# Performance work log

Measured on AMD Instinct MI355X. Metric: run time of the kernel, lower is better.

The kernel has to match this reference:

```python
import jax, jax.numpy as jnp
import numpy as np

N_OUT = 4096
N_IN = 4096
FRAC_SPARSE = 0.5
N_SPARSE = int(FRAC_SPARSE * N_OUT * N_IN)  # 8388608
TOKENS = 256


def setup_inputs() -> dict:
    key = jax.random.key(0)
    k1, k2 = jax.random.split(key)
    # x: activations fed to F.linear
    x = jax.random.normal(k1, (TOKENS, N_IN), dtype=jnp.float32)
    # sparse_values: nn.Parameter of size n_sparse
    sparse_values = jax.random.normal(k2, (N_SPARSE,), dtype=jnp.float32) * 0.02
    # sparse_mask as sorted unique row-major flat indices of True entries.
    # torch `out[mask] = values` fills values into True positions in row-major
    # order, which equals scattering values at the ascending-sorted flat idxs.
    rng = np.random.default_rng(0)
    flat_idx = np.sort(rng.permutation(N_OUT * N_IN)[:N_SPARSE]).astype(np.int32)
    return {"x": x, "sparse_values": sparse_values, "flat_idx": jnp.asarray(flat_idx)}


def reference(x, sparse_values, flat_idx):
    # reconstruct(): dense [n_out, n_in] weight via scatter of sparse values
    W = (
        jnp.zeros((N_OUT * N_IN,), dtype=sparse_values.dtype)
        .at[flat_idx]
        .set(sparse_values)
        .reshape(N_OUT, N_IN)
    )
    # F.linear(x, W) == x @ W.T
    return x @ W.T
```

## Files before the change

### kernel.cpp

```cpp
#include <hip/hip_runtime.h>
#include <stdint.h>

#define N_OUT    4096
#define N_IN     4096
#define TOKENS   256
#define N_SPARSE 8388608
#define SPLITK   16
#define KCHUNK   256
#define NSEG     (N_IN / KCHUNK)
#define CPW      (NSEG + 1)
#define BN       64

typedef __attribute__((ext_vector_type(8))) short bf16x8;
typedef __attribute__((ext_vector_type(8))) unsigned short u16x8;
typedef __attribute__((ext_vector_type(4))) float f32x4;

__device__ __forceinline__ unsigned short f2bf(float f) {
    union { float f; unsigned u; } v; v.f = f;
    unsigned r = v.u + 0x7fffu + ((v.u >> 16) & 1u);
    return (unsigned short)(r >> 16);
}

__device__ __forceinline__ float bf2f(unsigned short u) {
    union { unsigned u; float f; } v; v.u = ((unsigned)u) << 16;
    return v.f;
}

__device__ __forceinline__ void ld4(const int* __restrict__ idx,
                                    const float* __restrict__ vals,
                                    int jb, int4& i4, float4& v4) {
    if (jb + 4 <= N_SPARSE) {
        i4 = *(const int4*)(idx + jb);
        v4 = *(const float4*)(vals + jb);
    } else {
        i4 = int4{0, 0, 0, 0}; v4 = float4{0.f, 0.f, 0.f, 0.f};
        #pragma unroll
        for (int e = 0; e < 4; ++e) {
            const int j = jb + e;
            if (j < N_SPARSE) { (&i4.x)[e] = idx[j]; (&v4.x)[e] = vals[j]; }
        }
    }
}

__global__ void prep(const float* __restrict__ x, const int* __restrict__ idx,
                     unsigned short* __restrict__ xs, int* __restrict__ cp) {
    const int b = blockIdx.x;
    const int t = threadIdx.x;
    if (b < 1024) {
        const int i = (b * 256 + t) * 4;
        const int m = i >> 12;
        const int k = i & 4095;
        const float4 v = *(const float4*)(x + i);
        ushort4 o;
        o.x = f2bf(v.x); o.y = f2bf(v.y); o.z = f2bf(v.z); o.w = f2bf(v.w);
        const int lane = (m & 15) | (((k >> 3) & 3) << 4);
        const int addr = ((k >> 5) * 16 + (m >> 4)) * 512 + lane * 8 + (k & 7);
        *(ushort4*)(xs + addr) = o;
    } else {
        const int e = (b - 1024) * 256 + t;
        const int r = e / CPW;
        const int z = e - r * CPW;
        const int target = r * N_IN + z * KCHUNK;
        int lo = 0, hi = N_SPARSE;
        while (lo < hi) { int m = (lo + hi) >> 1; if (idx[m] < target) lo = m + 1; else hi = m; }
        cp[e] = lo;
    }
}

__global__ __launch_bounds__(256) void fused_gemm(
        const unsigned short* __restrict__ xs,
        const int* __restrict__ idx,
        const float* __restrict__ vals,
        const int* __restrict__ cp,
        unsigned short* __restrict__ part)
{
    __shared__ short Bs[BN * KCHUNK];

    const int tid = threadIdx.x;
    const int l   = tid & 63;
    const int w   = tid >> 6;
    const int bn  = blockIdx.x;
    const int bz  = blockIdx.y;

    {
        const u16x8 z8 = {};
        unsigned short* b0 = (unsigned short*)Bs + tid * 64;
        #pragma unroll
        for (int q = 0; q < 8; ++q) *(u16x8*)(b0 + q * 8) = z8;
    }
    __syncthreads();

    {
        const int rl    = tid >> 2;
        const int sub   = tid & 3;
        const int rglob = bn * BN + rl;
        const int start = cp[rglob * CPW + bz];
        const int end   = cp[rglob * CPW + bz + 1];
        const int base  = rglob * N_IN + bz * KCHUNK;
        unsigned short* brow = (unsigned short*)Bs + rl * KCHUNK;
        const int rx = (rl & 7) << 3;

        int jb = (start & ~3) + sub * 4;
        int4 i4; float4 v4;
        bool have = jb < end;
        if (have) ld4(idx, vals, jb, i4, v4);
        while (have) {
            const int jn = jb + 16;
            const bool haven = jn < end;
            int4 i4n; float4 v4n;
            if (haven) ld4(idx, vals, jn, i4n, v4n);
            #pragma unroll
            for (int e = 0; e < 4; ++e) {
                const int j = jb + e;
                if (j >= start && j < end) {
                    const int cc = (&i4.x)[e] - base;
                    brow[((cc & ~7) ^ rx) | (cc & 7)] = f2bf((&v4.x)[e]);
                }
            }
            jb = jn; i4 = i4n; v4 = v4n; have = haven;
        }
    }
    __syncthreads();

    const int lr  = l & 15;
    const int lkg = l >> 4;
    f32x4 acc[4][4] = {};
    const unsigned short* ax = xs + ((size_t)(bz * 8) * 16 + w * 4) * 512 + l * 8;

    #pragma unroll 2
    for (int kk = 0; kk < KCHUNK / 32; ++kk) {
        bf16x8 af[4], bfr[4];
        #pragma unroll
        for (int i = 0; i < 4; ++i)
            af[i] = *(const bf16x8*)(ax + (size_t)(kk * 16 + i) * 512);
        #pragma unroll
        for (int i = 0; i < 4; ++i) {
            const int n    = i * 16 + lr;
            const int slot = (kk * 4 + lkg) ^ (n & 7);
            bfr[i] = *(const bf16x8*)&Bs[n * KCHUNK + slot * 8];
        }
        #pragma unroll
        for (int mi = 0; mi < 4; ++mi)
            #pragma unroll
            for (int ni = 0; ni < 4; ++ni)
                acc[mi][ni] = __builtin_amdgcn_mfma_f32_16x16x32_bf16(
                                  af[mi], bfr[ni], acc[mi][ni], 0, 0, 0);
    }

    unsigned short* po = part + (size_t)bz * (TOKENS * N_OUT) + (size_t)bn * BN;
    #pragma unroll
    for (int mi = 0; mi < 4; ++mi)
        #pragma unroll
        for (int r = 0; r < 4; ++r) {
            const int m = w * 64 + mi * 16 + lkg * 4 + r;
            #pragma unroll
            for (int ni = 0; ni < 4; ++ni) {
                const int n = ni * 16 + lr;
                po[(size_t)m * N_OUT + n] = f2bf(acc[mi][ni][r]);
            }
        }
}

__global__ void reduce_k(const unsigned short* __restrict__ part, float* __restrict__ out) {
    const int i = (blockIdx.x * 256 + threadIdx.x) * 8;
    float a[8] = {};
    for (int z = 0; z < SPLITK; ++z) {
        const u16x8 p = *(const u16x8*)(part + (size_t)z * (TOKENS * N_OUT) + i);
        #pragma unroll
        for (int j = 0; j < 8; ++j) a[j] += bf2f((unsigned short)p[j]);
    }
    float4 o0 = { a[0], a[1], a[2], a[3] };
    float4 o1 = { a[4], a[5], a[6], a[7] };
    *(float4*)(out + i)     = o0;
    *(float4*)(out + i + 4) = o1;
}

__global__ void fallback_rowcsr(const float* __restrict__ x, const float* __restrict__ vals,
                                const int* __restrict__ idx, float* __restrict__ out) {
    const int o = blockIdx.x;
    const int t = threadIdx.x;
    __shared__ int   scol[256];
    __shared__ float sval[256];

    int lo = 0, hi = N_SPARSE;
    const int target = o * N_IN;
    while (lo < hi) { int m = (lo + hi) >> 1; if (idx[m] < target) lo = m + 1; else hi = m; }
    const int start = lo;
    hi = N_SPARSE;
    const int target2 = target + N_IN;
    while (lo < hi) { int m = (lo + hi) >> 1; if (idx[m] < target2) lo = m + 1; else hi = m; }
    const int end = lo;

    float acc = 0.f;
    const float* xr = x + (size_t)t * N_IN;
    for (int base = start; base < end; base += 256) {
        const int k = base + t;
        if (k < end) { scol[t] = idx[k] - target; sval[t] = vals[k]; }
        __syncthreads();
        const int cnt = min(256, end - base);
        for (int j = 0; j < cnt; ++j) acc += sval[j] * xr[scol[j]];
        __syncthreads();
    }
    out[(size_t)t * N_OUT + o] = acc;
}

extern "C" void kernel_launch(void* const* d_in, const int* in_sizes, int n_in,
                              void* d_out, int out_size, void* d_ws, size_t ws_size,
                              hipStream_t stream) {
    const float* x    = (const float*)d_in[0];
    const float* vals = (const float*)d_in[1];
    const int*   idx  = (const int*)d_in[2];
    float* out = (float*)d_out;

    const size_t part_bytes = (size_t)SPLITK * TOKENS * N_OUT * 2;
    const size_t xs_bytes   = (size_t)TOKENS * N_IN * 2;
    const size_t cp_bytes   = (size_t)N_OUT * CPW * 4;
    const size_t need = part_bytes + xs_bytes + cp_bytes;

    if (ws_size >= need) {
        unsigned short* part = (unsigned short*)d_ws;
        unsigned short* xs   = (unsigned short*)((char*)d_ws + part_bytes);
        int*            cp   = (int*)((char*)d_ws + part_bytes + xs_bytes);

        prep<<<1024 + (N_OUT * CPW) / 256, 256, 0, stream>>>(x, idx, xs, cp);
        dim3 grid(N_OUT / BN, SPLITK);
        fused_gemm<<<grid, 256, 0, stream>>>(xs, idx, vals, cp, part);
        reduce_k<<<(TOKENS * N_OUT) / 2048, 256, 0, stream>>>(part, out);
    } else {
        fallback_rowcsr<<<N_OUT, TOKENS, 0, stream>>>(x, vals, idx, out);
    }
}
```

Measured before the change: 56.37 us.

## Halve split-K, process two K chunks per block with 512 threads

Split-K drops from 16 to 8, and each block now loops over two 256-wide K segments. Blocks grow to 512 threads with 8 warps, each owning 32 token rows. The scatter loop keeps four independent index/value loads in flight per thread to hide global latency. This halves the bf16 partial-sum traffic written by the GEMM and read by the reduce. The cost is fewer blocks (512 instead of 1024) and extra barriers between chunks, since the shared B tile is reused without double buffering.

```diff
diff --git a/kernel.cpp b/kernel.cpp
--- a/kernel.cpp
+++ b/kernel.cpp
@@ -5,8 +5,9 @@
 #define N_IN     4096
 #define TOKENS   256
 #define N_SPARSE 8388608
-#define SPLITK   16
+#define SPLITK   8
 #define KCHUNK   256
+#define NCHUNK   2
 #define NSEG     (N_IN / KCHUNK)
 #define CPW      (NSEG + 1)
 #define BN       64
@@ -38,6 +39,19 @@
         for (int e = 0; e < 4; ++e) {
             const int j = jb + e;
             if (j < N_SPARSE) { (&i4.x)[e] = idx[j]; (&v4.x)[e] = vals[j]; }
+        }
+    }
+}
+
+__device__ __forceinline__ void consume4(const int4& i4, const float4& v4, int jb,
+                                         int start, int end, int base,
+                                         unsigned short* __restrict__ brow, int rx) {
+    #pragma unroll
+    for (int e = 0; e < 4; ++e) {
+        const int j = jb + e;
+        if (j >= start && j < end) {
+            const int cc = (&i4.x)[e] - base;
+            brow[((cc & ~7) ^ rx) | (cc & 7)] = f2bf((&v4.x)[e]);
         }
     }
 }
@@ -67,7 +81,7 @@
     }
 }
 
-__global__ __launch_bounds__(256) void fused_gemm(
+__global__ __launch_bounds__(512) void fused_gemm(
         const unsigned short* __restrict__ xs,
         const int* __restrict__ idx,
         const float* __restrict__ vals,
@@ -82,77 +96,88 @@
     const int bn  = blockIdx.x;
     const int bz  = blockIdx.y;
 
-    {
-        const u16x8 z8 = {};
-        unsigned short* b0 = (unsigned short*)Bs + tid * 64;
-        #pragma unroll
-        for (int q = 0; q < 8; ++q) *(u16x8*)(b0 + q * 8) = z8;
-    }
-    __syncthreads();
-
-    {
-        const int rl    = tid >> 2;
-        const int sub   = tid & 3;
-        const int rglob = bn * BN + rl;
-        const int start = cp[rglob * CPW + bz];
-        const int end   = cp[rglob * CPW + bz + 1];
-        const int base  = rglob * N_IN + bz * KCHUNK;
-        unsigned short* brow = (unsigned short*)Bs + rl * KCHUNK;
-        const int rx = (rl & 7) << 3;
-
-        int jb = (start & ~3) + sub * 4;
-        int4 i4; float4 v4;
-        bool have = jb < end;
-        if (have) ld4(idx, vals, jb, i4, v4);
-        while (have) {
-            const int jn = jb + 16;
-            const bool haven = jn < end;
-            int4 i4n; float4 v4n;
-            if (haven) ld4(idx, vals, jn, i4n, v4n);
-            #pragma unroll
-            for (int e = 0; e < 4; ++e) {
-                const int j = jb + e;
-                if (j >= start && j < end) {
-                    const int cc = (&i4.x)[e] - base;
-                    brow[((cc & ~7) ^ rx) | (cc & 7)] = f2bf((&v4.x)[e]);
+    const int rl    = tid >> 3;
+    const int sub   = tid & 7;
+    const int rglob = bn * BN + rl;
+    const int rx    = (rl & 7) << 3;
+    unsigned short* brow = (unsigned short*)Bs + rl * KCHUNK;
+
+    const int lr  = l & 15;
+    const int lkg = l >> 4;
+    f32x4 acc[2][4] = {};
+
+    #pragma unroll
+    for (int c = 0; c < NCHUNK; ++c) {
+        const int seg = bz * NCHUNK + c;
+
+        {
+            const u16x8 z8 = {};
+            unsigned short* b0 = (unsigned short*)Bs + tid * 32;
+            #pragma unroll
+            for (int q = 0; q < 4; ++q) *(u16x8*)(b0 + q * 8) = z8;
+        }
+        __syncthreads();
+
+        {
+            const int start = cp[rglob * CPW + seg];
+            const int end   = cp[rglob * CPW + seg + 1];
+            const int base  = rglob * N_IN + seg * KCHUNK;
+
+            int ja = (start & ~3) + sub * 4;
+            int jb_ = ja + 32, jc = ja + 64, jd = ja + 96;
+            int4 ia, ib, ic, id; float4 va, vb, vc, vd;
+            if (ja  < end) ld4(idx, vals, ja,  ia, va);
+            if (jb_ < end) ld4(idx, vals, jb_, ib, vb);
+            if (jc  < end) ld4(idx, vals, jc,  ic, vc);
+            if (jd  < end) ld4(idx, vals, jd,  id, vd);
+            while (ja < end) {
+                consume4(ia, va, ja, start, end, base, brow, rx);
+                ja += 128; if (ja < end) ld4(idx, vals, ja, ia, va);
+                if (jb_ < end) {
+                    consume4(ib, vb, jb_, start, end, base, brow, rx);
+                    jb_ += 128; if (jb_ < end) ld4(idx, vals, jb_, ib, vb);
+                }
+                if (jc < end) {
+                    consume4(ic, vc, jc, start, end, base, brow, rx);
+                    jc += 128; if (jc < end) ld4(idx, vals, jc, ic, vc);
+                }
+                if (jd < end) {
+                    consume4(id, vd, jd, start, end, base, brow, rx);
+                    jd += 128; if (jd < end) ld4(idx, vals, jd, id, vd);
                 }
             }
-            jb = jn; i4 = i4n; v4 = v4n; have = haven;
-        }
-    }
-    __syncthreads();
-
-    const int lr  = l & 15;
-    const int lkg = l >> 4;
-    f32x4 acc[4][4] = {};
-    const unsigned short* ax = xs + ((size_t)(bz * 8) * 16 + w * 4) * 512 + l * 8;
-
-    #pragma unroll 2
-    for (int kk = 0; kk < KCHUNK / 32; ++kk) {
-        bf16x8 af[4], bfr[4];
-        #pragma unroll
-        for (int i = 0; i < 4; ++i)
-            af[i] = *(const bf16x8*)(ax + (size_t)(kk * 16 + i) * 512);
-        #pragma unroll
-        for (int i = 0; i < 4; ++i) {
-            const int n    = i * 16 + lr;
-            const int slot = (kk * 4 + lkg) ^ (n & 7);
-            bfr[i] = *(const bf16x8*)&Bs[n * KCHUNK + slot * 8];
-        }
-        #pragma unroll
-        for (int mi = 0; mi < 4; ++mi)
-            #pragma unroll
-            for (int ni = 0; ni < 4; ++ni)
-                acc[mi][ni] = __builtin_amdgcn_mfma_f32_16x16x32_bf16(
-                                  af[mi], bfr[ni], acc[mi][ni], 0, 0, 0);
+        }
+        __syncthreads();
+
+        const unsigned short* ax = xs + ((size_t)(seg * 8) * 16) * 512 + l * 8;
+        #pragma unroll 2
+        for (int kk = 0; kk < KCHUNK / 32; ++kk) {
+            bf16x8 af[2], bfr[4];
+            #pragma unroll
+            for (int i = 0; i < 2; ++i)
+                af[i] = *(const bf16x8*)(ax + (size_t)(kk * 16 + w * 2 + i) * 512);
+            #pragma unroll
+            for (int i = 0; i < 4; ++i) {
+                const int n    = i * 16 + lr;
+                const int slot = (kk * 4 + lkg) ^ (n & 7);
+                bfr[i] = *(const bf16x8*)&Bs[n * KCHUNK + slot * 8];
+            }
+            #pragma unroll
+            for (int mi = 0; mi < 2; ++mi)
+                #pragma unroll
+                for (int ni = 0; ni < 4; ++ni)
+                    acc[mi][ni] = __builtin_amdgcn_mfma_f32_16x16x32_bf16(
+                                      af[mi], bfr[ni], acc[mi][ni], 0, 0, 0);
+        }
+        __syncthreads();
     }
 
     unsigned short* po = part + (size_t)bz * (TOKENS * N_OUT) + (size_t)bn * BN;
     #pragma unroll
-    for (int mi = 0; mi < 4; ++mi)
+    for (int mi = 0; mi < 2; ++mi)
         #pragma unroll
         for (int r = 0; r < 4; ++r) {
-            const int m = w * 64 + mi * 16 + lkg * 4 + r;
+            const int m = w * 32 + mi * 16 + lkg * 4 + r;
             #pragma unroll
             for (int ni = 0; ni < 4; ++ni) {
                 const int n = ni * 16 + lr;
@@ -224,7 +249,7 @@
 
         prep<<<1024 + (N_OUT * CPW) / 256, 256, 0, stream>>>(x, idx, xs, cp);
         dim3 grid(N_OUT / BN, SPLITK);
-        fused_gemm<<<grid, 256, 0, stream>>>(xs, idx, vals, cp, part);
+        fused_gemm<<<grid, 512, 0, stream>>>(xs, idx, vals, cp, part);
         reduce_k<<<(TOKENS * N_OUT) / 2048, 256, 0, stream>>>(part, out);
     } else {
         fallback_rowcsr<<<N_OUT, TOKENS, 0, stream>>>(x, vals, idx, out);
```

Result: faster. 45.68 us (-19.0%).

## Give each wave its own 16-row weight slice to drop block barriers

Applied to the files above, without the earlier changes.

Each wave now zeroes, scatters and consumes only its own 16 output rows of the shared weight tile, so both __syncthreads barriers go away. Each wave computes all 256 tokens against its 16 columns instead of a 64x64 quadrant. The scatter loop keeps four independent load streams in flight, and branchy stores are replaced by predicated writes that send out-of-range entries to a trash buffer. In exchange, every wave now reloads all 16 A fragments from global memory per k step, roughly quadrupling A traffic. The partial-sum output stores also become narrower per wave.

```diff
diff --git a/kernel.cpp b/kernel.cpp
--- a/kernel.cpp
+++ b/kernel.cpp
@@ -39,6 +39,20 @@
             const int j = jb + e;
             if (j < N_SPARSE) { (&i4.x)[e] = idx[j]; (&v4.x)[e] = vals[j]; }
         }
+    }
+}
+
+__device__ __forceinline__ void consume4(const int4& i4, const float4& v4, int jb,
+                                         int start, int end, int base,
+                                         unsigned short* __restrict__ brow, int rx,
+                                         unsigned short* __restrict__ trash) {
+    #pragma unroll
+    for (int e = 0; e < 4; ++e) {
+        const int j  = jb + e;
+        const int cc = (&i4.x)[e] - base;
+        unsigned short* p = (j >= start && j < end)
+                          ? &brow[((cc & ~7) ^ rx) | (cc & 7)] : trash;
+        *p = f2bf((&v4.x)[e]);
     }
 }
 
@@ -74,7 +88,8 @@
         const int* __restrict__ cp,
         unsigned short* __restrict__ part)
 {
-    __shared__ short Bs[BN * KCHUNK];
+    __shared__ unsigned short Bs[4][16 * KCHUNK];
+    __shared__ unsigned short trash[32];
 
     const int tid = threadIdx.x;
     const int l   = tid & 63;
@@ -82,82 +97,74 @@
     const int bn  = blockIdx.x;
     const int bz  = blockIdx.y;
 
+    unsigned short* bsw = &Bs[w][0];
+
     {
         const u16x8 z8 = {};
-        unsigned short* b0 = (unsigned short*)Bs + tid * 64;
-        #pragma unroll
-        for (int q = 0; q < 8; ++q) *(u16x8*)(b0 + q * 8) = z8;
-    }
-    __syncthreads();
+        #pragma unroll
+        for (int q = 0; q < 8; ++q)
+            *(u16x8*)(bsw + q * 512 + l * 8) = z8;
+    }
 
     {
-        const int rl    = tid >> 2;
-        const int sub   = tid & 3;
-        const int rglob = bn * BN + rl;
+        const int rs    = l >> 2;
+        const int sub   = l & 3;
+        const int rglob = bn * BN + w * 16 + rs;
         const int start = cp[rglob * CPW + bz];
         const int end   = cp[rglob * CPW + bz + 1];
         const int base  = rglob * N_IN + bz * KCHUNK;
-        unsigned short* brow = (unsigned short*)Bs + rl * KCHUNK;
-        const int rx = (rl & 7) << 3;
-
-        int jb = (start & ~3) + sub * 4;
-        int4 i4; float4 v4;
-        bool have = jb < end;
-        if (have) ld4(idx, vals, jb, i4, v4);
-        while (have) {
-            const int jn = jb + 16;
-            const bool haven = jn < end;
-            int4 i4n; float4 v4n;
-            if (haven) ld4(idx, vals, jn, i4n, v4n);
-            #pragma unroll
-            for (int e = 0; e < 4; ++e) {
-                const int j = jb + e;
-                if (j >= start && j < end) {
-                    const int cc = (&i4.x)[e] - base;
-                    brow[((cc & ~7) ^ rx) | (cc & 7)] = f2bf((&v4.x)[e]);
-                }
+        const int rx    = (rs & 7) << 3;
+        unsigned short* brow = bsw + rs * KCHUNK;
+
+        int ja  = (start & ~3) + sub * 4;
+        int jb_ = ja + 16, jc = ja + 32, jd = ja + 48;
+        int4 ia, ib, ic, id; float4 va, vb, vc, vd;
+        if (ja  < end) ld4(idx, vals, ja,  ia, va);
+        if (jb_ < end) ld4(idx, vals, jb_, ib, vb);
+        if (jc  < end) ld4(idx, vals, jc,  ic, vc);
+        if (jd  < end) ld4(idx, vals, jd,  id, vd);
+        while (ja < end) {
+            consume4(ia, va, ja, start, end, base, brow, rx, trash);
+            ja += 64; if (ja < end) ld4(idx, vals, ja, ia, va);
+            if (jb_ < end) {
+                consume4(ib, vb, jb_, start, end, base, brow, rx, trash);
+                jb_ += 64; if (jb_ < end) ld4(idx, vals, jb_, ib, vb);
             }
-            jb = jn; i4 = i4n; v4 = v4n; have = haven;
-        }
-    }
-    __syncthreads();
+            if (jc < end) {
+                consume4(ic, vc, jc, start, end, base, brow, rx, trash);
+                jc += 64; if (jc < end) ld4(idx, vals, jc, ic, vc);
+            }
+            if (jd < end) {
+                consume4(id, vd, jd, start, end, base, brow, rx, trash);
+                jd += 64; if (jd < end) ld4(idx, vals, jd, id, vd);
+            }
+        }
+    }
 
     const int lr  = l & 15;
     const int lkg = l >> 4;
-    f32x4 acc[4][4] = {};
-    const unsigned short* ax = xs + ((size_t)(bz * 8) * 16 + w * 4) * 512 + l * 8;
+    f32x4 acc[16] = {};
+    const unsigned short* ax = xs + (size_t)(bz * 8 * 16) * 512 + l * 8;
 
     #pragma unroll 2
     for (int kk = 0; kk < KCHUNK / 32; ++kk) {
-        bf16x8 af[4], bfr[4];
-        #pragma unroll
-        for (int i = 0; i < 4; ++i)
-            af[i] = *(const bf16x8*)(ax + (size_t)(kk * 16 + i) * 512);
-        #pragma unroll
-        for (int i = 0; i < 4; ++i) {
-            const int n    = i * 16 + lr;
-            const int slot = (kk * 4 + lkg) ^ (n & 7);
-            bfr[i] = *(const bf16x8*)&Bs[n * KCHUNK + slot * 8];
-        }
-        #pragma unroll
-        for (int mi = 0; mi < 4; ++mi)
-            #pragma unroll
-            for (int ni = 0; ni < 4; ++ni)
-                acc[mi][ni] = __builtin_amdgcn_mfma_f32_16x16x32_bf16(
-                                  af[mi], bfr[ni], acc[mi][ni], 0, 0, 0);
-    }
-
-    unsigned short* po = part + (size_t)bz * (TOKENS * N_OUT) + (size_t)bn * BN;
+        const bf16x8 bfr = *(const bf16x8*)
+            &bsw[lr * KCHUNK + (((kk * 4 + lkg) ^ (lr & 7)) << 3)];
+        #pragma unroll
+        for (int mf = 0; mf < 16; ++mf) {
+            const bf16x8 af = *(const bf16x8*)(ax + (size_t)(kk * 16 + mf) * 512);
+            acc[mf] = __builtin_amdgcn_mfma_f32_16x16x32_bf16(af, bfr, acc[mf], 0, 0, 0);
+        }
+    }
+
+    unsigned short* po = part + (size_t)bz * (TOKENS * N_OUT)
+                              + (size_t)bn * BN + w * 16 + lr;
     #pragma unroll
-    for (int mi = 0; mi < 4; ++mi)
+    for (int mf = 0; mf < 16; ++mf)
         #pragma unroll
         for (int r = 0; r < 4; ++r) {
-            const int m = w * 64 + mi * 16 + lkg * 4 + r;
-            #pragma unroll
-            for (int ni = 0; ni < 4; ++ni) {
-                const int n = ni * 16 + lr;
-                po[(size_t)m * N_OUT + n] = f2bf(acc[mi][ni][r]);
-            }
+            const int m = mf * 16 + lkg * 4 + r;
+            po[(size_t)m * N_OUT] = f2bf(acc[mf][r]);
         }
 }
 
```

After: 102.5 us. 1.82x slower.

## Materialize dense bf16 weight, then run split-K GEMM with async LDS double buffering

Applied to the files above, without the earlier changes.

The sparse scatter moves out of the GEMM into a separate build_w kernel. It rebuilds each weight row in shared memory and writes a dense bf16 W to workspace, using row pointers found by a binary search in a narrowed window. The GEMM then streams W tiles into LDS with global_load_lds, double-buffered across four K chunks. Split-K drops from 16 to 4, which cuts partial-sum traffic and reduce work. The cost is an extra 32MB write and read of W. The narrowed search window also assumes each row holds about half density, which may not hold for other masks.

```diff
diff --git a/kernel.cpp b/kernel.cpp
--- a/kernel.cpp
+++ b/kernel.cpp
@@ -5,11 +5,10 @@
 #define N_IN     4096
 #define TOKENS   256
 #define N_SPARSE 8388608
-#define SPLITK   16
+#define SPLITK   4
+#define BN       64
+#define KSPAN    (N_IN / SPLITK)
 #define KCHUNK   256
-#define NSEG     (N_IN / KCHUNK)
-#define CPW      (NSEG + 1)
-#define BN       64
 
 typedef __attribute__((ext_vector_type(8))) short bf16x8;
 typedef __attribute__((ext_vector_type(8))) unsigned short u16x8;
@@ -24,6 +23,12 @@
 __device__ __forceinline__ float bf2f(unsigned short u) {
     union { unsigned u; float f; } v; v.u = ((unsigned)u) << 16;
     return v.f;
+}
+
+__device__ __forceinline__ void gload_lds16(const void* g, void* l) {
+    __builtin_amdgcn_global_load_lds(
+        (const __attribute__((address_space(1))) void*)g,
+        (__attribute__((address_space(3))) void*)l, 16, 0, 0);
 }
 
 __device__ __forceinline__ void ld4(const int* __restrict__ idx,
@@ -43,7 +48,7 @@
 }
 
 __global__ void prep(const float* __restrict__ x, const int* __restrict__ idx,
-                     unsigned short* __restrict__ xs, int* __restrict__ cp) {
+                     unsigned short* __restrict__ xs, int* __restrict__ rp) {
     const int b = blockIdx.x;
     const int t = threadIdx.x;
     if (b < 1024) {
@@ -57,24 +62,87 @@
         const int addr = ((k >> 5) * 16 + (m >> 4)) * 512 + lane * 8 + (k & 7);
         *(ushort4*)(xs + addr) = o;
     } else {
-        const int e = (b - 1024) * 256 + t;
-        const int r = e / CPW;
-        const int z = e - r * CPW;
-        const int target = r * N_IN + z * KCHUNK;
-        int lo = 0, hi = N_SPARSE;
-        while (lo < hi) { int m = (lo + hi) >> 1; if (idx[m] < target) lo = m + 1; else hi = m; }
-        cp[e] = lo;
-    }
-}
-
-__global__ __launch_bounds__(256) void fused_gemm(
+        const int r = (b - 1024) * 256 + t;
+        if (r > N_OUT) return;
+        const int target = r << 12;
+        const int c = r << 11;
+        int lo = c > 16384 ? c - 16384 : 0;
+        int hi = c + 16384 < N_SPARSE ? c + 16384 : N_SPARSE;
+        while (lo < hi) {
+            const int m = (lo + hi) >> 1;
+            if (idx[m] < target) lo = m + 1; else hi = m;
+        }
+        rp[r] = lo;
+    }
+}
+
+__global__ __launch_bounds__(256) void build_w(const int* __restrict__ idx,
+                                               const float* __restrict__ vals,
+                                               const int* __restrict__ rp,
+                                               unsigned short* __restrict__ wb) {
+    __shared__ unsigned short row[N_IN];
+    const int r = blockIdx.x;
+    const int t = threadIdx.x;
+    const int base = r << 12;
+
+    {
+        const u16x8 z8 = {};
+        *(u16x8*)&row[t * 16]     = z8;
+        *(u16x8*)&row[t * 16 + 8] = z8;
+    }
+    const int start = rp[r];
+    const int end   = rp[r + 1];
+    __syncthreads();
+
+    {
+        int jb = (start & ~3) + t * 4;
+        int4 ia, ib, ic; float4 va, vb, vc;
+        const bool ha = jb < end, hb = jb + 1024 < end, hc = jb + 2048 < end;
+        if (ha) ld4(idx, vals, jb,        ia, va);
+        if (hb) ld4(idx, vals, jb + 1024, ib, vb);
+        if (hc) ld4(idx, vals, jb + 2048, ic, vc);
+        #pragma unroll
+        for (int e = 0; e < 4; ++e) {
+            const int j = jb + e;
+            if (j >= start && j < end) row[(&ia.x)[e] - base] = f2bf((&va.x)[e]);
+        }
+        if (hb) {
+            #pragma unroll
+            for (int e = 0; e < 4; ++e) {
+                const int j = jb + 1024 + e;
+                if (j < end) row[(&ib.x)[e] - base] = f2bf((&vb.x)[e]);
+            }
+        }
+        if (hc) {
+            #pragma unroll
+            for (int e = 0; e < 4; ++e) {
+                const int j = jb + 2048 + e;
+                if (j < end) row[(&ic.x)[e] - base] = f2bf((&vc.x)[e]);
+            }
+        }
+        for (jb += 3072; jb < end; jb += 1024) {
+            int4 i4; float4 v4;
+            ld4(idx, vals, jb, i4, v4);
+            #pragma unroll
+            for (int e = 0; e < 4; ++e) {
+                const int j = jb + e;
+                if (j < end) row[(&i4.x)[e] - base] = f2bf((&v4.x)[e]);
+            }
+        }
+    }
+    __syncthreads();
+
+    unsigned short* wo = wb + (size_t)base + t * 16;
+    *(u16x8*)wo       = *(const u16x8*)&row[t * 16];
+    *(u16x8*)(wo + 8) = *(const u16x8*)&row[t * 16 + 8];
+}
+
+__global__ __launch_bounds__(512) void gemm_bt(
         const unsigned short* __restrict__ xs,
-        const int* __restrict__ idx,
-        const float* __restrict__ vals,
-        const int* __restrict__ cp,
+        const unsigned short* __restrict__ wb,
         unsigned short* __restrict__ part)
 {
-    __shared__ short Bs[BN * KCHUNK];
+    __shared__ short Bs[2][BN * KCHUNK];
 
     const int tid = threadIdx.x;
     const int l   = tid & 63;
@@ -82,77 +150,69 @@
     const int bn  = blockIdx.x;
     const int bz  = blockIdx.y;
 
-    {
-        const u16x8 z8 = {};
-        unsigned short* b0 = (unsigned short*)Bs + tid * 64;
-        #pragma unroll
-        for (int q = 0; q < 8; ++q) *(u16x8*)(b0 + q * 8) = z8;
-    }
-    __syncthreads();
-
-    {
-        const int rl    = tid >> 2;
-        const int sub   = tid & 3;
-        const int rglob = bn * BN + rl;
-        const int start = cp[rglob * CPW + bz];
-        const int end   = cp[rglob * CPW + bz + 1];
-        const int base  = rglob * N_IN + bz * KCHUNK;
-        unsigned short* brow = (unsigned short*)Bs + rl * KCHUNK;
-        const int rx = (rl & 7) << 3;
-
-        int jb = (start & ~3) + sub * 4;
-        int4 i4; float4 v4;
-        bool have = jb < end;
-        if (have) ld4(idx, vals, jb, i4, v4);
-        while (have) {
-            const int jn = jb + 16;
-            const bool haven = jn < end;
-            int4 i4n; float4 v4n;
-            if (haven) ld4(idx, vals, jn, i4n, v4n);
-            #pragma unroll
-            for (int e = 0; e < 4; ++e) {
-                const int j = jb + e;
-                if (j >= start && j < end) {
-                    const int cc = (&i4.x)[e] - base;
-                    brow[((cc & ~7) ^ rx) | (cc & 7)] = f2bf((&v4.x)[e]);
-                }
-            }
-            jb = jn; i4 = i4n; v4 = v4n; have = haven;
-        }
-    }
+    const int srow  = tid >> 5;
+    const int sslot = tid & 31;
+    const unsigned short* wbase = wb + (size_t)(bn * BN) * N_IN + bz * KSPAN;
+
+#define STAGE(tt, bb) do { \
+        _Pragma("unroll") \
+        for (int rnd = 0; rnd < 4; ++rnd) { \
+            const int row = rnd * 16 + srow; \
+            gload_lds16(wbase + (size_t)row * N_IN + (tt) * KCHUNK \
+                              + ((sslot ^ (row & 7)) * 8), \
+                        &Bs[bb][rnd * 4096 + tid * 8]); \
+        } } while (0)
+
+    STAGE(0, 0);
     __syncthreads();
 
     const int lr  = l & 15;
     const int lkg = l >> 4;
-    f32x4 acc[4][4] = {};
-    const unsigned short* ax = xs + ((size_t)(bz * 8) * 16 + w * 4) * 512 + l * 8;
-
-    #pragma unroll 2
-    for (int kk = 0; kk < KCHUNK / 32; ++kk) {
-        bf16x8 af[4], bfr[4];
-        #pragma unroll
-        for (int i = 0; i < 4; ++i)
-            af[i] = *(const bf16x8*)(ax + (size_t)(kk * 16 + i) * 512);
-        #pragma unroll
-        for (int i = 0; i < 4; ++i) {
-            const int n    = i * 16 + lr;
-            const int slot = (kk * 4 + lkg) ^ (n & 7);
-            bfr[i] = *(const bf16x8*)&Bs[n * KCHUNK + slot * 8];
-        }
-        #pragma unroll
-        for (int mi = 0; mi < 4; ++mi)
-            #pragma unroll
-            for (int ni = 0; ni < 4; ++ni)
-                acc[mi][ni] = __builtin_amdgcn_mfma_f32_16x16x32_bf16(
-                                  af[mi], bfr[ni], acc[mi][ni], 0, 0, 0);
-    }
+    f32x4 acc[2][4] = {};
+
+    #pragma unroll
+    for (int t = 0; t < 4; ++t) {
+        const int cur = t & 1;
+        const int seg = bz * 4 + t;
+
+        bf16x8 afr[16];
+        {
+            const unsigned short* ax = xs + (size_t)(seg * 128) * 512 + l * 8;
+            #pragma unroll
+            for (int q = 0; q < 16; ++q)
+                afr[q] = *(const bf16x8*)(ax + (size_t)((q >> 1) * 16 + w * 2 + (q & 1)) * 512);
+        }
+        if (t + 1 < 4) STAGE(t + 1, cur ^ 1);
+
+        {
+            const short* bsc = &Bs[cur][0];
+            #pragma unroll
+            for (int kk = 0; kk < KCHUNK / 32; ++kk) {
+                bf16x8 bfr[4];
+                #pragma unroll
+                for (int i = 0; i < 4; ++i) {
+                    const int n    = i * 16 + lr;
+                    const int slot = (kk * 4 + lkg) ^ (n & 7);
+                    bfr[i] = *(const bf16x8*)&bsc[n * KCHUNK + slot * 8];
+                }
+                #pragma unroll
+                for (int mi = 0; mi < 2; ++mi)
+                    #pragma unroll
+                    for (int ni = 0; ni < 4; ++ni)
+                        acc[mi][ni] = __builtin_amdgcn_mfma_f32_16x16x32_bf16(
+                                          afr[kk * 2 + mi], bfr[ni], acc[mi][ni], 0, 0, 0);
+            }
+        }
+        __syncthreads();
+    }
+#undef STAGE
 
     unsigned short* po = part + (size_t)bz * (TOKENS * N_OUT) + (size_t)bn * BN;
     #pragma unroll
-    for (int mi = 0; mi < 4; ++mi)
+    for (int mi = 0; mi < 2; ++mi)
         #pragma unroll
         for (int r = 0; r < 4; ++r) {
-            const int m = w * 64 + mi * 16 + lkg * 4 + r;
+            const int m = w * 32 + mi * 16 + lkg * 4 + r;
             #pragma unroll
             for (int ni = 0; ni < 4; ++ni) {
                 const int n = ni * 16 + lr;
@@ -214,17 +274,20 @@
 
     const size_t part_bytes = (size_t)SPLITK * TOKENS * N_OUT * 2;
     const size_t xs_bytes   = (size_t)TOKENS * N_IN * 2;
-    const size_t cp_bytes   = (size_t)N_OUT * CPW * 4;
-    const size_t need = part_bytes + xs_bytes + cp_bytes;
+    const size_t wb_bytes   = (size_t)N_OUT * N_IN * 2;
+    const size_t rp_bytes   = (size_t)(N_OUT + 1) * 4;
+    const size_t need = part_bytes + xs_bytes + wb_bytes + rp_bytes;
 
     if (ws_size >= need) {
         unsigned short* part = (unsigned short*)d_ws;
         unsigned short* xs   = (unsigned short*)((char*)d_ws + part_bytes);
-        int*            cp   = (int*)((char*)d_ws + part_bytes + xs_bytes);
-
-        prep<<<1024 + (N_OUT * CPW) / 256, 256, 0, stream>>>(x, idx, xs, cp);
+        unsigned short* wb   = (unsigned short*)((char*)d_ws + part_bytes + xs_bytes);
+        int*            rp   = (int*)((char*)d_ws + part_bytes + xs_bytes + wb_bytes);
+
+        prep<<<1024 + 17, 256, 0, stream>>>(x, idx, xs, rp);
+        build_w<<<N_OUT, 256, 0, stream>>>(idx, vals, rp, wb);
         dim3 grid(N_OUT / BN, SPLITK);
-        fused_gemm<<<grid, 256, 0, stream>>>(xs, idx, vals, cp, part);
+        gemm_bt<<<grid, 512, 0, stream>>>(xs, wb, part);
         reduce_k<<<(TOKENS * N_OUT) / 2048, 256, 0, stream>>>(part, out);
     } else {
         fallback_rowcsr<<<N_OUT, TOKENS, 0, stream>>>(x, vals, idx, out);
```

Result: no change. 55.80 us (median of 2 runs) (-1.0%).
